# Kernel optimization log

Measured on AMD Instinct MI355X. Metric: run time of the kernel, lower is better.

Reference implementation:

```python
import jax, jax.numpy as jnp
import numpy as np

NQ = 4          # n_qubits -> 2**4 = 16 amplitudes
NL = 3          # n_layers
TWO_PI = 2.0 * np.pi
BN_EPS = 1e-5


def _ry_batched(t):
    # t: [B] -> [B,2,2] complex64
    c, s = jnp.cos(t / 2), jnp.sin(t / 2)
    g = jnp.stack([jnp.stack([c, -s], -1), jnp.stack([s, c], -1)], -2)
    return g.astype(jnp.complex64)


def _ry(t):
    c, s = jnp.cos(t / 2), jnp.sin(t / 2)
    return jnp.stack([jnp.stack([c, -s]), jnp.stack([s, c])]).astype(jnp.complex64)


def _rz(t):
    e = jnp.stack([jnp.exp(-0.5j * t), jnp.exp(0.5j * t)]).astype(jnp.complex64)
    return jnp.diag(e)


def _apply_1q(state, gate, wire, batched):
    # state: [B,2,2,2,2]; gate: [2,2] or [B,2,2]
    s = jnp.moveaxis(state, wire + 1, -1)
    if batched:
        s = jnp.einsum('bij,b...j->b...i', gate, s)
    else:
        s = jnp.einsum('ij,...j->...i', gate, s)
    return jnp.moveaxis(s, -1, wire + 1)


def _apply_cnot(state, c, t):
    s = jnp.moveaxis(state, (c + 1, t + 1), (-2, -1))
    s = jnp.stack([s[..., 0, :], s[..., 1, ::-1]], axis=-2)  # flip target when control=1
    return jnp.moveaxis(s, (-2, -1), (c + 1, t + 1))


def _circuit(angles, weights):
    # angles: [B, NQ] float32; weights: [NL, NQ, 2]
    B = angles.shape[0]
    state = jnp.zeros((B,) + (2,) * NQ, jnp.complex64)
    state = state.at[(slice(None),) + (0,) * NQ].set(1.0)
    # input encoding RYs (per-sample angles -> batched gates)
    for i in range(NQ):
        state = _apply_1q(state, _ry_batched(angles[:, i]), i, True)
    for layer in range(NL):
        for i in range(NQ):
            state = _apply_1q(state, _ry(weights[layer, i, 0]), i, False)
            state = _apply_1q(state, _rz(weights[layer, i, 1]), i, False)
        for i in range(NQ - 1):
            state = _apply_cnot(state, i, i + 1)
        state = _apply_cnot(state, NQ - 1, 0)
    probs = jnp.abs(state) ** 2  # [B,2,2,2,2] real
    zs = []
    for i in range(NQ):
        axes = tuple(a for a in range(1, NQ + 1) if a != i + 1)
        pm = probs.sum(axis=axes)  # [B,2]
        zs.append(pm[:, 0] - pm[:, 1])
    return jnp.stack(zs, -1).astype(jnp.float32)  # [B,NQ]


def setup_inputs() -> dict:
    key = jax.random.key(0)
    ks = jax.random.split(key, 4)
    B = 524288
    x = jax.random.normal(ks[0], (B, 16), jnp.float32)
    weights = jax.random.normal(ks[1], (NL, NQ, 2), jnp.float32)
    fc_w = jax.random.normal(ks[2], (4, NQ), jnp.float32) / np.sqrt(NQ)
    fc_b = jax.random.normal(ks[3], (4,), jnp.float32) * 0.01
    gamma = jnp.ones((4,), jnp.float32)
    beta = jnp.zeros((4,), jnp.float32)
    return {"x": x, "weights": weights, "fc_w": fc_w, "fc_b": fc_b,
            "gamma": gamma, "beta": beta}


def reference(x, weights, fc_w, fc_b, gamma, beta):
    inp = x.reshape(x.shape[0], -1)[:, :NQ]
    mn, mx = inp.min(), inp.max()  # global min/max as in the torch code
    angles = TWO_PI * (inp - mn) / (mx - mn + 1e-8)
    q = _circuit(angles, weights)                # [B,4] PauliZ expvals
    out = q @ fc_w.T + fc_b                      # Linear(4,4)
    mean = out.mean(0)
    var = out.var(0)                             # biased, as torch BN training
    return gamma * (out - mean) / jnp.sqrt(var + BN_EPS) + beta
```

## Files before the change

kernel.cpp:

```cpp
#include <hip/hip_runtime.h>
#include <hip/hip_cooperative_groups.h>
#include <math.h>

namespace cg = cooperative_groups;

#define TWO_PI_F 6.28318530717958647692f
#define BN_EPS_F 1e-5f

#define NBLK 1024
#define NT 256

#define NB1 2048
#define NB2 1024

#define MKEY_OFF 0
#define STAT_OFF 4
#define CTAB_OFF 16
#define BMIN_OFF 256
#define BMAX_OFF 2304
#define TAB_OFF 4352
#define SSLOT_OFF 4992

__device__ __forceinline__ unsigned fkey(float f) {
  unsigned u = __float_as_uint(f);
  return u ^ (unsigned(int(u) >> 31) | 0x80000000u);
}
__device__ __forceinline__ float funkey(unsigned k) {
  unsigned u = (k & 0x80000000u) ? (k ^ 0x80000000u) : ~k;
  return __uint_as_float(u);
}

__device__ __forceinline__ void build_ucol(int col, const float* __restrict__ w,
                                           float* sr, float* si) {
#pragma unroll
  for (int k = 0; k < 16; ++k) { sr[k] = (k == col) ? 1.f : 0.f; si[k] = 0.f; }
#pragma unroll
  for (int l = 0; l < 3; ++l) {
#pragma unroll
    for (int i = 0; i < 4; ++i) {
      const int m = 8 >> i;
      float ryc, rys, rzc, rzs;
      __sincosf(0.5f * w[(l * 4 + i) * 2 + 0], &rys, &ryc);
      __sincosf(0.5f * w[(l * 4 + i) * 2 + 1], &rzs, &rzc);
#pragma unroll
      for (int k = 0; k < 16; ++k) {
        if (!(k & m)) {
          int k1 = k | m;
          float a0r = sr[k], a0i = si[k], a1r = sr[k1], a1i = si[k1];
          sr[k] = ryc * a0r - rys * a1r;
          si[k] = ryc * a0i - rys * a1i;
          sr[k1] = rys * a0r + ryc * a1r;
          si[k1] = rys * a0i + ryc * a1i;
        }
      }
#pragma unroll
      for (int k = 0; k < 16; ++k) {
        float ps = (k & m) ? rzs : -rzs;
        float rr = sr[k], ii = si[k];
        sr[k] = rr * rzc - ii * ps;
        si[k] = rr * ps + ii * rzc;
      }
    }
#pragma unroll
    for (int c = 0; c < 4; ++c) {
      const int mc = 8 >> c;
      const int mt = 8 >> ((c + 1) & 3);
#pragma unroll
      for (int k = 0; k < 16; ++k) {
        if ((k & mc) && !(k & mt)) {
          int k2 = k | mt;
          float tt;
          tt = sr[k]; sr[k] = sr[k2]; sr[k2] = tt;
          tt = si[k]; si[k] = si[k2]; si[k2] = tt;
        }
      }
    }
  }
}

__global__ __launch_bounds__(128) void k0_init(const float* __restrict__ w,
                                               const float* __restrict__ fc_w,
                                               float* __restrict__ wsf) {
  int tid = threadIdx.x;
  if (tid < 16) {
    float sr[16], si[16];
    build_ucol(tid, w, sr, si);
#pragma unroll
    for (int k = 0; k < 16; ++k) {
      wsf[CTAB_OFF + tid * 16 + k] = sr[k];
      wsf[CTAB_OFF + 256 + tid * 16 + k] = si[k];
    }
  } else if (tid < 24) {
    wsf[STAT_OFF + (tid - 16)] = 0.f;
  } else if (tid == 24) {
    unsigned* mk = (unsigned*)wsf + MKEY_OFF;
    mk[0] = 0xFFFFFFFFu;
    mk[1] = 0u;
  } else if (tid >= 64 && tid < 128) {
    int e = tid - 64, k = e >> 2, j = e & 3;
    float s = 0.f;
#pragma unroll
    for (int i = 0; i < 4; ++i)
      s += fc_w[j * 4 + i] * ((k & (8 >> i)) ? -1.f : 1.f);
    wsf[CTAB_OFF + 512 + k * 4 + j] = s;
  }
}

__device__ __forceinline__ void qfc_one(const float* __restrict__ tab,
                                        const float* c, const float* s,
                                        float* o) {
  const float* __restrict__ Ur = tab;
  const float* __restrict__ Ui = tab + 256;
  const float* __restrict__ At = tab + 512;
  float A01[4] = {c[0] * c[1], c[0] * s[1], s[0] * c[1], s[0] * s[1]};
  float A23[4] = {c[2] * c[3], c[2] * s[3], s[2] * c[3], s[2] * s[3]};
  float yr[16], yi[16];
#pragma unroll
  for (int k = 0; k < 16; ++k) { yr[k] = yi[k] = 0.f; }
#pragma unroll
  for (int a = 0; a < 16; ++a) {
    float va = A01[a >> 2] * A23[a & 3];
#pragma unroll
    for (int k = 0; k < 16; ++k) {
      yr[k] = fmaf(Ur[a * 16 + k], va, yr[k]);
      yi[k] = fmaf(Ui[a * 16 + k], va, yi[k]);
    }
  }
#pragma unroll
  for (int j = 0; j < 4; ++j) o[j] = 0.f;
#pragma unroll
  for (int k = 0; k < 16; ++k) {
    float p = fmaf(yr[k], yr[k], yi[k] * yi[k]);
#pragma unroll
    for (int j = 0; j < 4; ++j) o[j] = fmaf(At[k * 4 + j], p, o[j]);
  }
}

__global__ __launch_bounds__(NT, 4) void fused(
    const float* __restrict__ x, unsigned* __restrict__ mk,
    float* __restrict__ stp, const float* __restrict__ tab,
    const float* __restrict__ gamma, const float* __restrict__ beta,
    float* __restrict__ out, int B) {
  const int tid = threadIdx.x;
  const int gtid = blockIdx.x * NT + tid;
  const int H = NBLK * NT;
  const int wv = tid >> 6, ln = tid & 63;
  __shared__ float smn[4], smx[4];
  __shared__ float red[4][8];
  __shared__ float sbc[2];
  __shared__ float sst[8];

  const int s0 = gtid, s1 = gtid + H;
  const bool h0 = s0 < B, h1 = s1 < B;
  float4 xa = h0 ? *(const float4*)(x + (size_t)s0 * 16) : make_float4(0, 0, 0, 0);
  float4 xb = h1 ? *(const float4*)(x + (size_t)s1 * 16) : make_float4(0, 0, 0, 0);

  float fmn = __builtin_inff(), fmx = -__builtin_inff();
  if (h0) {
    fmn = fminf(fminf(xa.x, xa.y), fminf(xa.z, xa.w));
    fmx = fmaxf(fmaxf(xa.x, xa.y), fmaxf(xa.z, xa.w));
  }
  if (h1) {
    fmn = fminf(fmn, fminf(fminf(xb.x, xb.y), fminf(xb.z, xb.w)));
    fmx = fmaxf(fmx, fmaxf(fmaxf(xb.x, xb.y), fmaxf(xb.z, xb.w)));
  }
#pragma unroll
  for (int d = 32; d; d >>= 1) {
    fmn = fminf(fmn, __shfl_down(fmn, d));
    fmx = fmaxf(fmx, __shfl_down(fmx, d));
  }
  if (ln == 0) { smn[wv] = fmn; smx[wv] = fmx; }
  __syncthreads();
  if (tid == 0) {
    float bm = fminf(fminf(smn[0], smn[1]), fminf(smn[2], smn[3]));
    float bM = fmaxf(fmaxf(smx[0], smx[1]), fmaxf(smx[2], smx[3]));
    atomicMin(mk + 0, fkey(bm));
    atomicMax(mk + 1, fkey(bM));
  }

  cg::this_grid().sync();

  if (tid == 0) {
    unsigned kmin = __hip_atomic_load(mk + 0, __ATOMIC_RELAXED,
                                      __HIP_MEMORY_SCOPE_AGENT);
    unsigned kmax = __hip_atomic_load(mk + 1, __ATOMIC_RELAXED,
                                      __HIP_MEMORY_SCOPE_AGENT);
    sbc[0] = funkey(kmin);
    sbc[1] = funkey(kmax);
  }
  __syncthreads();
  const float gm = sbc[0], gM = sbc[1];
  const float ssc = TWO_PI_F * 0.5f / (gM - gm + 1e-8f);

  float a0[4] = {xa.x, xa.y, xa.z, xa.w};
  float a1[4] = {xb.x, xb.y, xb.z, xb.w};
  float c0[4], sn0[4], c1[4], sn1[4];
#pragma unroll
  for (int i = 0; i < 4; ++i) {
    __sincosf((a0[i] - gm) * ssc, &sn0[i], &c0[i]);
    __sincosf((a1[i] - gm) * ssc, &sn1[i], &c1[i]);
  }
  float o0[4], o1[4];
  qfc_one(tab, c0, sn0, o0);
  qfc_one(tab, c1, sn1, o1);

  float vals[8];
#pragma unroll
  for (int j = 0; j < 4; ++j) {
    float v0 = h0 ? o0[j] : 0.f, v1 = h1 ? o1[j] : 0.f;
    vals[j] = v0 + v1;
    vals[4 + j] = fmaf(v0, v0, v1 * v1);
  }
#pragma unroll
  for (int j = 0; j < 8; ++j) {
#pragma unroll
    for (int d = 32; d; d >>= 1) vals[j] += __shfl_down(vals[j], d);
  }
  if (ln == 0) {
#pragma unroll
    for (int j = 0; j < 8; ++j) red[wv][j] = vals[j];
  }
  __syncthreads();
  if (tid < 8)
    atomicAdd(stp + tid, red[0][tid] + red[1][tid] + red[2][tid] + red[3][tid]);

  cg::this_grid().sync();

  if (tid < 8)
    sst[tid] = __hip_atomic_load(stp + tid, __ATOMIC_RELAXED,
                                 __HIP_MEMORY_SCOPE_AGENT);
  __syncthreads();

  const float inv = 1.0f / (float)B;
  float sc[4], sh[4];
#pragma unroll
  for (int j = 0; j < 4; ++j) {
    float mean = sst[j] * inv;
    float var = sst[4 + j] * inv - mean * mean;
    float is = rsqrtf(var + BN_EPS_F);
    sc[j] = gamma[j] * is;
    sh[j] = beta[j] - mean * sc[j];
  }
  if (h0)
    *(float4*)(out + (size_t)s0 * 4) =
        make_float4(fmaf(o0[0], sc[0], sh[0]), fmaf(o0[1], sc[1], sh[1]),
                    fmaf(o0[2], sc[2], sh[2]), fmaf(o0[3], sc[3], sh[3]));
  if (h1)
    *(float4*)(out + (size_t)s1 * 4) =
        make_float4(fmaf(o1[0], sc[0], sh[0]), fmaf(o1[1], sc[1], sh[1]),
                    fmaf(o1[2], sc[2], sh[2]), fmaf(o1[3], sc[3], sh[3]));
}

__global__ __launch_bounds__(NT) void k1_scan_tab(const float* __restrict__ x,
                                                  const float* __restrict__ w,
                                                  const float* __restrict__ fc_w,
                                                  float* __restrict__ wsf, int B) {
  int r = blockIdx.x * NT + threadIdx.x;
  float fmn = __builtin_inff(), fmx = -__builtin_inff();
  if (r < B) {
    float4 v = *(const float4*)(x + (size_t)r * 16);
    fmn = fminf(fminf(v.x, v.y), fminf(v.z, v.w));
    fmx = fmaxf(fmaxf(v.x, v.y), fmaxf(v.z, v.w));
  }
#pragma unroll
  for (int d = 32; d; d >>= 1) {
    fmn = fminf(fmn, __shfl_down(fmn, d));
    fmx = fmaxf(fmx, __shfl_down(fmx, d));
  }
  __shared__ float smn[4], smx[4];
  int wv = threadIdx.x >> 6, ln = threadIdx.x & 63;
  if (ln == 0) { smn[wv] = fmn; smx[wv] = fmx; }
  __syncthreads();
  if (threadIdx.x == 0) {
    wsf[BMIN_OFF + blockIdx.x] =
        fminf(fminf(smn[0], smn[1]), fminf(smn[2], smn[3]));
    wsf[BMAX_OFF + blockIdx.x] =
        fmaxf(fmaxf(smx[0], smx[1]), fmaxf(smx[2], smx[3]));
  }
  if (blockIdx.x == 0) {
    int tid = threadIdx.x;
    if (tid < 16) {
      float sr[16], si[16];
      build_ucol(tid, w, sr, si);
#pragma unroll
      for (int k = 0; k < 16; ++k) {
        wsf[TAB_OFF + tid * 16 + k] = sr[k];
        wsf[TAB_OFF + 256 + tid * 16 + k] = si[k];
      }
    } else if (tid == 16) {
      for (int k = 0; k < 16; ++k)
        for (int j = 0; j < 4; ++j) {
          float s = 0.f;
          for (int i = 0; i < 4; ++i)
            s += fc_w[j * 4 + i] * ((k & (8 >> i)) ? -1.f : 1.f);
          wsf[TAB_OFF + 512 + k * 4 + j] = s;
        }
    }
  }
}

__device__ __forceinline__ void qfc_pair(const float* __restrict__ tab,
                                         const float* c0, const float* s0,
                                         const float* c1, const float* s1,
                                         float* o0, float* o1) {
  const float* __restrict__ Ur = tab;
  const float* __restrict__ Ui = tab + 256;
  const float* __restrict__ At = tab + 512;
  float A01_0[4] = {c0[0] * c0[1], c0[0] * s0[1], s0[0] * c0[1], s0[0] * s0[1]};
  float A23_0[4] = {c0[2] * c0[3], c0[2] * s0[3], s0[2] * c0[3], s0[2] * s0[3]};
  float A01_1[4] = {c1[0] * c1[1], c1[0] * s1[1], s1[0] * c1[1], s1[0] * s1[1]};
  float A23_1[4] = {c1[2] * c1[3], c1[2] * s1[3], s1[2] * c1[3], s1[2] * s1[3]};
  float yr0[16], yi0[16], yr1[16], yi1[16];
#pragma unroll
  for (int k = 0; k < 16; ++k) { yr0[k] = yi0[k] = yr1[k] = yi1[k] = 0.f; }
#pragma unroll
  for (int a = 0; a < 16; ++a) {
    float va0 = A01_0[a >> 2] * A23_0[a & 3];
    float va1 = A01_1[a >> 2] * A23_1[a & 3];
#pragma unroll
    for (int k = 0; k < 16; ++k) {
      float ur = Ur[a * 16 + k], ui = Ui[a * 16 + k];
      yr0[k] = fmaf(ur, va0, yr0[k]);
      yi0[k] = fmaf(ui, va0, yi0[k]);
      yr1[k] = fmaf(ur, va1, yr1[k]);
      yi1[k] = fmaf(ui, va1, yi1[k]);
    }
  }
#pragma unroll
  for (int j = 0; j < 4; ++j) { o0[j] = 0.f; o1[j] = 0.f; }
#pragma unroll
  for (int k = 0; k < 16; ++k) {
    float p0 = fmaf(yr0[k], yr0[k], yi0[k] * yi0[k]);
    float p1 = fmaf(yr1[k], yr1[k], yi1[k] * yi1[k]);
#pragma unroll
    for (int j = 0; j < 4; ++j) {
      float av = At[k * 4 + j];
      o0[j] = fmaf(av, p0, o0[j]);
      o1[j] = fmaf(av, p1, o1[j]);
    }
  }
}

__global__ __launch_bounds__(NT) void k2_main(const float* __restrict__ x,
                                              const float* __restrict__ wsf,
                                              float* __restrict__ sslot,
                                              float* __restrict__ out, int B) {
  const int tid = threadIdx.x;
  const int gtid = blockIdx.x * NT + tid;
  const int H = NB2 * NT;
  const int wv = tid >> 6, ln = tid & 63;
  const float* __restrict__ tab = wsf + TAB_OFF;

  float gm = __builtin_inff(), gM = -__builtin_inff();
#pragma unroll
  for (int q = 0; q < NB1 / 64; ++q) {
    int i = ln + q * 64;
    gm = fminf(gm, wsf[BMIN_OFF + i]);
    gM = fmaxf(gM, wsf[BMAX_OFF + i]);
  }
#pragma unroll
  for (int d = 32; d; d >>= 1) {
    gm = fminf(gm, __shfl_down(gm, d));
    gM = fmaxf(gM, __shfl_down(gM, d));
  }
  gm = __shfl(gm, 0);
  gM = __shfl(gM, 0);
  const float ssc = TWO_PI_F * 0.5f / (gM - gm + 1e-8f);

  const int s0 = gtid, s1 = gtid + H;
  const bool h0 = s0 < B, h1 = s1 < B;
  float4 xa = h0 ? *(const float4*)(x + (size_t)s0 * 16) : make_float4(0, 0, 0, 0);
  float4 xb = h1 ? *(const float4*)(x + (size_t)s1 * 16) : make_float4(0, 0, 0, 0);

  float a0[4] = {xa.x, xa.y, xa.z, xa.w};
  float a1[4] = {xb.x, xb.y, xb.z, xb.w};
  float c0[4], sn0[4], c1[4], sn1[4];
#pragma unroll
  for (int i = 0; i < 4; ++i) {
    __sincosf((a0[i] - gm) * ssc, &sn0[i], &c0[i]);
    __sincosf((a1[i] - gm) * ssc, &sn1[i], &c1[i]);
  }
  float o0[4], o1[4];
  qfc_pair(tab, c0, sn0, c1, sn1, o0, o1);

  if (h0)
    *(float4*)(out + (size_t)s0 * 4) = make_float4(o0[0], o0[1], o0[2], o0[3]);
  if (h1)
    *(float4*)(out + (size_t)s1 * 4) = make_float4(o1[0], o1[1], o1[2], o1[3]);

  float vals[8];
#pragma unroll
  for (int j = 0; j < 4; ++j) {
    float v0 = h0 ? o0[j] : 0.f, v1 = h1 ? o1[j] : 0.f;
    vals[j] = v0 + v1;
    vals[4 + j] = fmaf(v0, v0, v1 * v1);
  }
#pragma unroll
  for (int j = 0; j < 8; ++j) {
#pragma unroll
    for (int d = 32; d; d >>= 1) vals[j] += __shfl_down(vals[j], d);
  }
  __shared__ float red[4][8];
  if (ln == 0) {
#pragma unroll
    for (int j = 0; j < 8; ++j) red[wv][j] = vals[j];
  }
  __syncthreads();
  if (tid < 8) {
    sslot[blockIdx.x * 8 + tid] =
        red[0][tid] + red[1][tid] + red[2][tid] + red[3][tid];
  }
}

__global__ __launch_bounds__(NT) void k3_final(float* __restrict__ out,
                                               const float* __restrict__ sslot,
                                               const float* __restrict__ gamma,
                                               const float* __restrict__ beta,
                                               int B) {
  const int tid = threadIdx.x;
  const int gtid = blockIdx.x * NT + tid;
  const int H = NB2 * NT;
  const int ln = tid & 63;

  float v = 0.f;
#pragma unroll
  for (int k = 0; k < (NB2 * 8) / 64; ++k) v += sslot[k * 64 + ln];
#pragma unroll
  for (int d = 32; d >= 8; d >>= 1) v += __shfl_down(v, d);
  float st[8];
#pragma unroll
  for (int j = 0; j < 8; ++j) st[j] = __shfl(v, j);

  const float inv = 1.0f / (float)B;
  float sc[4], sh[4];
#pragma unroll
  for (int j = 0; j < 4; ++j) {
    float mean = st[j] * inv;
    float var = st[4 + j] * inv - mean * mean;
    float is = rsqrtf(var + BN_EPS_F);
    sc[j] = gamma[j] * is;
    sh[j] = beta[j] - mean * sc[j];
  }
#pragma unroll
  for (int p = 0; p < 2; ++p) {
    int s = gtid + p * H;
    if (s < B) {
      float4 q = *(float4*)(out + (size_t)s * 4);
      *(float4*)(out + (size_t)s * 4) =
          make_float4(fmaf(q.x, sc[0], sh[0]), fmaf(q.y, sc[1], sh[1]),
                      fmaf(q.z, sc[2], sh[2]), fmaf(q.w, sc[3], sh[3]));
    }
  }
}

extern "C" void kernel_launch(void* const* d_in, const int* in_sizes, int n_in,
                              void* d_out, int out_size, void* d_ws, size_t ws_size,
                              hipStream_t stream) {
  const float* x = (const float*)d_in[0];
  const float* w = (const float*)d_in[1];
  const float* fc_w = (const float*)d_in[2];
  const float* gamma = (const float*)d_in[4];
  const float* beta = (const float*)d_in[5];
  float* out = (float*)d_out;
  float* wsf = (float*)d_ws;
  int B = in_sizes[0] / 16;

  k0_init<<<1, 128, 0, stream>>>(w, fc_w, wsf);

  static int coop_state = -1;
  if (coop_state < 0) {
    int dev = 0;
    (void)hipGetDevice(&dev);
    int coop = 0;
    (void)hipDeviceGetAttribute(&coop, hipDeviceAttributeCooperativeLaunch, dev);
    int ncu = 0;
    (void)hipDeviceGetAttribute(&ncu, hipDeviceAttributeMultiprocessorCount, dev);
    int per_cu = 0;
    (void)hipOccupancyMaxActiveBlocksPerMultiprocessor(&per_cu,
                                                       (const void*)fused, NT, 0);
    coop_state = (coop && ncu > 0 && per_cu > 0 &&
                  (long long)per_cu * ncu >= NBLK)
                     ? 1
                     : 0;
  }

  hipError_t e = hipErrorUnknown;
  if (coop_state == 1 && B <= 2 * NBLK * NT) {
    unsigned* mk = (unsigned*)wsf + MKEY_OFF;
    float* stp = wsf + STAT_OFF;
    const float* tab = wsf + CTAB_OFF;
    void* args[] = {(void*)&x,     (void*)&mk,   (void*)&stp, (void*)&tab,
                    (void*)&gamma, (void*)&beta, (void*)&out, (void*)&B};
    e = hipLaunchCooperativeKernel((const void*)fused, dim3(NBLK), dim3(NT),
                                   args, 0, stream);
    if (e != hipSuccess) {
      (void)hipGetLastError();
      coop_state = 0;
    }
  }
  if (e != hipSuccess) {
    k1_scan_tab<<<NB1, NT, 0, stream>>>(x, w, fc_w, wsf, B);
    k2_main<<<NB2, NT, 0, stream>>>(x, wsf, wsf + SSLOT_OFF, out, B);
    k3_final<<<NB2, NT, 0, stream>>>(out, wsf + SSLOT_OFF, gamma, beta, B);
  }
}
```

Measured before the change: 116.8 us.

## Replace cooperative grid sync with custom hierarchical atomic barrier and sharded reductions

Drops the cooperative launch and cg grid sync in favour of a normal launch with a two-level atomic barrier (32 leaves of 32 blocks, then a root flag broadcast). The min/max keys and BN statistic accumulators are spread across padded shards so fewer blocks contend on one address, and each block reduces the shards afterwards with wave shuffles. This targets cooperative launch overhead, barrier latency and atomic contention. The catch is that forward progress depends on all 1024 blocks being co-resident, which is only checked through the occupancy query, so a wrong estimate would deadlock.

Measured after the change: 118.4 us. About the same (+1.4%).

```diff
diff --git a/kernel.cpp b/kernel.cpp
--- a/kernel.cpp
+++ b/kernel.cpp
@@ -1,21 +1,28 @@
 #include <hip/hip_runtime.h>
-#include <hip/hip_cooperative_groups.h>
 #include <math.h>
-
-namespace cg = cooperative_groups;
 
 #define TWO_PI_F 6.28318530717958647692f
 #define BN_EPS_F 1e-5f
 
 #define NBLK 1024
 #define NT 256
+#define NLEAF 32
+#define MKSH 16
+#define STSH 64
 
 #define NB1 2048
 #define NB2 1024
 
-#define MKEY_OFF 0
-#define STAT_OFF 4
-#define CTAB_OFF 16
+#define MK_OFF 0
+#define LEAFA_OFF 512
+#define FLAGA_OFF 1536
+#define ROOTA_OFF 2560
+#define LEAFB_OFF 2592
+#define FLAGB_OFF 3616
+#define ROOTB_OFF 4640
+#define UZERO_N 5696
+#define STAT_OFF 4672
+#define CTAB_OFF 5696
 #define BMIN_OFF 256
 #define BMAX_OFF 2304
 #define TAB_OFF 4352
@@ -82,6 +89,9 @@
                                                const float* __restrict__ fc_w,
                                                float* __restrict__ wsf) {
   int tid = threadIdx.x;
+  unsigned* u = (unsigned*)wsf;
+  for (int i = tid; i < UZERO_N; i += 128) u[i] = 0u;
+  __syncthreads();
   if (tid < 16) {
     float sr[16], si[16];
     build_ucol(tid, w, sr, si);
@@ -90,12 +100,8 @@
       wsf[CTAB_OFF + tid * 16 + k] = sr[k];
       wsf[CTAB_OFF + 256 + tid * 16 + k] = si[k];
     }
-  } else if (tid < 24) {
-    wsf[STAT_OFF + (tid - 16)] = 0.f;
-  } else if (tid == 24) {
-    unsigned* mk = (unsigned*)wsf + MKEY_OFF;
-    mk[0] = 0xFFFFFFFFu;
-    mk[1] = 0u;
+  } else if (tid < 32) {
+    u[MK_OFF + (tid - 16) * 32] = 0xFFFFFFFFu;
   } else if (tid >= 64 && tid < 128) {
     int e = tid - 64, k = e >> 2, j = e & 3;
     float s = 0.f;
@@ -104,6 +110,31 @@
       s += fc_w[j * 4 + i] * ((k & (8 >> i)) ? -1.f : 1.f);
     wsf[CTAB_OFF + 512 + k * 4 + j] = s;
   }
+}
+
+__device__ __forceinline__ void grid_barrier(unsigned* __restrict__ leaf,
+                                             unsigned* __restrict__ flag,
+                                             unsigned* __restrict__ root) {
+  __syncthreads();
+  if (threadIdx.x == 0) {
+    const int l = (int)(blockIdx.x >> 5);
+    unsigned p = __hip_atomic_fetch_add(leaf + l * 32, 1u, __ATOMIC_ACQ_REL,
+                                        __HIP_MEMORY_SCOPE_AGENT);
+    if (p == 31u) {
+      unsigned q = __hip_atomic_fetch_add(root, 1u, __ATOMIC_ACQ_REL,
+                                          __HIP_MEMORY_SCOPE_AGENT);
+      if (q == (unsigned)(NLEAF - 1)) {
+#pragma unroll
+        for (int f = 0; f < NLEAF; ++f)
+          __hip_atomic_store(flag + f * 32, 1u, __ATOMIC_RELEASE,
+                             __HIP_MEMORY_SCOPE_AGENT);
+      }
+    }
+    while (__hip_atomic_load(flag + l * 32, __ATOMIC_ACQUIRE,
+                             __HIP_MEMORY_SCOPE_AGENT) == 0u)
+      __builtin_amdgcn_s_sleep(2);
+  }
+  __syncthreads();
 }
 
 __device__ __forceinline__ void qfc_one(const float* __restrict__ tab,
@@ -137,18 +168,18 @@
 }
 
 __global__ __launch_bounds__(NT, 4) void fused(
-    const float* __restrict__ x, unsigned* __restrict__ mk,
-    float* __restrict__ stp, const float* __restrict__ tab,
+    const float* __restrict__ x, float* __restrict__ wsf,
     const float* __restrict__ gamma, const float* __restrict__ beta,
     float* __restrict__ out, int B) {
   const int tid = threadIdx.x;
   const int gtid = blockIdx.x * NT + tid;
   const int H = NBLK * NT;
   const int wv = tid >> 6, ln = tid & 63;
+  unsigned* __restrict__ u = (unsigned*)wsf;
+  const float* __restrict__ tab = wsf + CTAB_OFF;
+  float* __restrict__ stat = wsf + STAT_OFF;
   __shared__ float smn[4], smx[4];
   __shared__ float red[4][8];
-  __shared__ float sbc[2];
-  __shared__ float sst[8];
 
   const int s0 = gtid, s1 = gtid + H;
   const bool h0 = s0 < B, h1 = s1 < B;
@@ -174,22 +205,29 @@
   if (tid == 0) {
     float bm = fminf(fminf(smn[0], smn[1]), fminf(smn[2], smn[3]));
     float bM = fmaxf(fmaxf(smx[0], smx[1]), fmaxf(smx[2], smx[3]));
-    atomicMin(mk + 0, fkey(bm));
-    atomicMax(mk + 1, fkey(bM));
-  }
-
-  cg::this_grid().sync();
-
-  if (tid == 0) {
-    unsigned kmin = __hip_atomic_load(mk + 0, __ATOMIC_RELAXED,
-                                      __HIP_MEMORY_SCOPE_AGENT);
-    unsigned kmax = __hip_atomic_load(mk + 1, __ATOMIC_RELAXED,
-                                      __HIP_MEMORY_SCOPE_AGENT);
-    sbc[0] = funkey(kmin);
-    sbc[1] = funkey(kmax);
-  }
-  __syncthreads();
-  const float gm = sbc[0], gM = sbc[1];
+    const int sh = (int)(blockIdx.x & (MKSH - 1));
+    atomicMin(u + MK_OFF + sh * 32, fkey(bm));
+    atomicMax(u + MK_OFF + sh * 32 + 16, fkey(bM));
+  }
+
+  grid_barrier(u + LEAFA_OFF, u + FLAGA_OFF, u + ROOTA_OFF);
+
+  unsigned km = 0xFFFFFFFFu, kM = 0u;
+  if (ln < MKSH) {
+    km = __hip_atomic_load(u + MK_OFF + ln * 32, __ATOMIC_RELAXED,
+                           __HIP_MEMORY_SCOPE_AGENT);
+    kM = __hip_atomic_load(u + MK_OFF + ln * 32 + 16, __ATOMIC_RELAXED,
+                           __HIP_MEMORY_SCOPE_AGENT);
+  }
+#pragma unroll
+  for (int d = 8; d; d >>= 1) {
+    unsigned tm = __shfl_down(km, d), tM = __shfl_down(kM, d);
+    km = (tm < km) ? tm : km;
+    kM = (tM > kM) ? tM : kM;
+  }
+  km = __shfl(km, 0);
+  kM = __shfl(kM, 0);
+  const float gm = funkey(km), gM = funkey(kM);
   const float ssc = TWO_PI_F * 0.5f / (gM - gm + 1e-8f);
 
   float a0[4] = {xa.x, xa.y, xa.z, xa.w};
@@ -221,22 +259,30 @@
     for (int j = 0; j < 8; ++j) red[wv][j] = vals[j];
   }
   __syncthreads();
-  if (tid < 8)
-    atomicAdd(stp + tid, red[0][tid] + red[1][tid] + red[2][tid] + red[3][tid]);
-
-  cg::this_grid().sync();
-
-  if (tid < 8)
-    sst[tid] = __hip_atomic_load(stp + tid, __ATOMIC_RELAXED,
-                                 __HIP_MEMORY_SCOPE_AGENT);
-  __syncthreads();
+  if (tid < 8) {
+    const int sh = (int)(blockIdx.x & (STSH - 1));
+    atomicAdd(stat + sh * 16 + tid,
+              red[0][tid] + red[1][tid] + red[2][tid] + red[3][tid]);
+  }
+
+  grid_barrier(u + LEAFB_OFF, u + FLAGB_OFF, u + ROOTB_OFF);
+
+  float st[8];
+#pragma unroll
+  for (int j = 0; j < 8; ++j) {
+    float v = __hip_atomic_load(stat + ln * 16 + j, __ATOMIC_RELAXED,
+                                __HIP_MEMORY_SCOPE_AGENT);
+#pragma unroll
+    for (int d = 32; d; d >>= 1) v += __shfl_down(v, d);
+    st[j] = __shfl(v, 0);
+  }
 
   const float inv = 1.0f / (float)B;
   float sc[4], sh[4];
 #pragma unroll
   for (int j = 0; j < 4; ++j) {
-    float mean = sst[j] * inv;
-    float var = sst[4 + j] * inv - mean * mean;
+    float mean = st[j] * inv;
+    float var = st[4 + j] * inv - mean * mean;
     float is = rsqrtf(var + BN_EPS_F);
     sc[j] = gamma[j] * is;
     sh[j] = beta[j] - mean * sc[j];
@@ -471,34 +517,18 @@
   if (coop_state < 0) {
     int dev = 0;
     (void)hipGetDevice(&dev);
-    int coop = 0;
-    (void)hipDeviceGetAttribute(&coop, hipDeviceAttributeCooperativeLaunch, dev);
     int ncu = 0;
     (void)hipDeviceGetAttribute(&ncu, hipDeviceAttributeMultiprocessorCount, dev);
     int per_cu = 0;
     (void)hipOccupancyMaxActiveBlocksPerMultiprocessor(&per_cu,
                                                        (const void*)fused, NT, 0);
-    coop_state = (coop && ncu > 0 && per_cu > 0 &&
-                  (long long)per_cu * ncu >= NBLK)
-                     ? 1
-                     : 0;
-  }
-
-  hipError_t e = hipErrorUnknown;
+    coop_state =
+        (ncu > 0 && per_cu > 0 && (long long)per_cu * ncu >= NBLK) ? 1 : 0;
+  }
+
   if (coop_state == 1 && B <= 2 * NBLK * NT) {
-    unsigned* mk = (unsigned*)wsf + MKEY_OFF;
-    float* stp = wsf + STAT_OFF;
-    const float* tab = wsf + CTAB_OFF;
-    void* args[] = {(void*)&x,     (void*)&mk,   (void*)&stp, (void*)&tab,
-                    (void*)&gamma, (void*)&beta, (void*)&out, (void*)&B};
-    e = hipLaunchCooperativeKernel((const void*)fused, dim3(NBLK), dim3(NT),
-                                   args, 0, stream);
-    if (e != hipSuccess) {
-      (void)hipGetLastError();
-      coop_state = 0;
-    }
-  }
-  if (e != hipSuccess) {
+    fused<<<NBLK, NT, 0, stream>>>(x, wsf, gamma, beta, out, B);
+  } else {
     k1_scan_tab<<<NB1, NT, 0, stream>>>(x, w, fc_w, wsf, B);
     k2_main<<<NB2, NT, 0, stream>>>(x, wsf, wsf + SSLOT_OFF, out, B);
     k3_final<<<NB2, NT, 0, stream>>>(out, wsf + SSLOT_OFF, gamma, beta, B);
```
